# Kernel tuning notes

Hardware: AMD Instinct MI355X
Metric: run time of the kernel (lower is better)

## Reference

```python
import jax, jax.numpy as jnp
import numpy as np

B, S, D = 4, 2048, 1024
H, HD = 16, 64  # nb_heads, head_size


def setup_inputs() -> dict:
    key = jax.random.key(0)
    ks = jax.random.split(key, 9)
    s = 1.0 / np.sqrt(D)
    return {
        "x": jax.random.normal(ks[0], (B, S, D), dtype=jnp.float32),
        "wq": jax.random.uniform(ks[1], (D, D), jnp.float32, -s, s),
        "bq": jax.random.uniform(ks[2], (D,), jnp.float32, -s, s),
        "wk": jax.random.uniform(ks[3], (D, D), jnp.float32, -s, s),
        "bk": jax.random.uniform(ks[4], (D,), jnp.float32, -s, s),
        "wv": jax.random.uniform(ks[5], (D, D), jnp.float32, -s, s),
        "bv": jax.random.uniform(ks[6], (D,), jnp.float32, -s, s),
        "wo": jax.random.uniform(ks[7], (D, D), jnp.float32, -s, s),
        "bo": jax.random.uniform(ks[8], (D,), jnp.float32, -s, s),
    }


def _split_heads(t):
    # [B,S,D] -> [B,H,S,HD]
    return t.reshape(B, S, H, HD).transpose(0, 2, 1, 3)


def reference(x, wq, bq, wk, bk, wv, bv, wo, bo):
    q = _split_heads(x @ wq + bq)
    k = _split_heads(x @ wk + bk)
    v = _split_heads(x @ wv + bv)
    scores = jnp.einsum("bhqd,bhkd->bhqk", q, k) / jnp.sqrt(jnp.float32(HD))
    causal = jnp.tril(jnp.ones((S, S), dtype=bool))
    scores = jnp.where(causal, scores, -jnp.inf)
    w = jax.nn.softmax(scores, axis=-1)
    a = jnp.einsum("bhqk,bhkd->bhqd", w, v)
    a = a.transpose(0, 2, 1, 3).reshape(B, S, D)
    return a @ wo + bo
```

## Files before the change

### kernel.cpp

```cpp
#include <hip/hip_runtime.h>
#include <hip/hip_bf16.h>

typedef __bf16 bf16;
typedef bf16 bf16x8 __attribute__((ext_vector_type(8)));
typedef float f32x4 __attribute__((ext_vector_type(4)));
typedef unsigned short u16;

#define B_ 4
#define S_ 2048
#define D_ 1024
#define H_ 16
#define HD_ 64

#define NEG_SENT -30000.0f

#define XN_OFF   ((size_t)0)
#define WT_OFF   ((size_t)8388608)
#define BN_OFF   ((size_t)12582912)
#define FLAG_BYTE ((size_t)25174016)
#define Q_OFF    ((size_t)12587520)
#define K_OFF    ((size_t)20976128)
#define VT_OFF   ((size_t)29364736)

union Pack4 { bf16 b[4]; uint2 q; };

__device__ __forceinline__ void load16(const bf16* g, bf16* l) {
    __builtin_amdgcn_global_load_lds(
        (const __attribute__((address_space(1))) void*)g,
        (__attribute__((address_space(3))) void*)l, 16, 0, 0);
}

__global__ __launch_bounds__(256) void preproc_k(
    const void* __restrict__ x,
    const void* __restrict__ W0, const void* __restrict__ W1,
    const void* __restrict__ W2, const void* __restrict__ W3,
    const void* __restrict__ b0, const void* __restrict__ b1,
    const void* __restrict__ b2, const void* __restrict__ b3,
    bf16* __restrict__ XN, bf16* __restrict__ WT, bf16* __restrict__ BN,
    int* __restrict__ flag)
{
    __shared__ __align__(16) bf16 tile[64][65];
    __shared__ int cnt;
    const int t = threadIdx.x;
    const int bid = blockIdx.x;

    if (t == 0) cnt = 0;
    __syncthreads();
    {
        const u16* xs = (const u16*)x;
        int c = 0;
        for (int i = t; i < 4096; i += 256) {
            u16 w = xs[i * 2];
            int e = (w >> 7) & 0xFF;
            if (e >= 100 && e <= 135) c++;
        }
        atomicAdd(&cnt, c);
    }
    __syncthreads();
    const int isb = (cnt > 2048) ? 1 : 0;

    if (bid < 2048) {
        for (int qi = bid * 256 + t; qi < 2097152; qi += 2048 * 256) {
            if (isb) {
                ((uint2*)XN)[qi] = ((const uint2*)x)[qi];
            } else {
                float4 v = ((const float4*)x)[qi];
                Pack4 p;
                p.b[0] = (bf16)v.x; p.b[1] = (bf16)v.y;
                p.b[2] = (bf16)v.z; p.b[3] = (bf16)v.w;
                ((uint2*)XN)[qi] = p.q;
            }
        }
    } else if (bid < 3072) {
        const int idx = bid - 2048;
        const int mat = idx >> 8;
        const int rem = idx & 255;
        const int r0 = ((rem >> 4) & 15) * 64, c0 = (rem & 15) * 64;
        const void* W = (mat == 0) ? W0 : (mat == 1) ? W1
                        : (mat == 2) ? W2 : W3;
        bf16* O = WT + ((size_t)mat << 20);
        #pragma unroll
        for (int i = 0; i < 16; ++i) {
            int id2 = t + i * 256;
            int r = id2 >> 6, c = id2 & 63;
            size_t off = (size_t)(r0 + r) * D_ + c0 + c;
            tile[r][c] = isb ? ((const bf16*)W)[off]
                             : (bf16)((const float*)W)[off];
        }
        __syncthreads();
        #pragma unroll
        for (int i = 0; i < 16; ++i) {
            int id2 = t + i * 256;
            int rr = id2 & 63, cc = id2 >> 6;
            O[(size_t)(c0 + cc) * D_ + r0 + rr] = tile[rr][cc];
        }
    } else {
        if (t == 0) *flag = isb;
        const int i = t * 4;
        #pragma unroll
        for (int mat = 0; mat < 4; ++mat) {
            const void* src = (mat == 0) ? b0 : (mat == 1) ? b1
                              : (mat == 2) ? b2 : b3;
            bf16* dst = BN + mat * 1024;
            if (isb) {
                ((uint2*)(dst + i))[0] = *(const uint2*)((const bf16*)src + i);
            } else {
                const float* s = (const float*)src;
                Pack4 p;
                p.b[0] = (bf16)s[i + 0]; p.b[1] = (bf16)s[i + 1];
                p.b[2] = (bf16)s[i + 2]; p.b[3] = (bf16)s[i + 3];
                ((uint2*)(dst + i))[0] = p.q;
            }
        }
    }
}

__device__ __forceinline__ void gemm_core(const bf16* __restrict__ A,
                                          const bf16* __restrict__ Bt,
                                          bf16* lA, bf16* lB,
                                          f32x4 acc[4][4], int m0, int n0)
{
    const int t = threadIdx.x;
    const int lane = t & 63;
    const int wave = t >> 6;
    const int wm = (wave >> 1) << 6;
    const int wn = (wave & 1) << 6;
    const int quad = lane >> 4;
    const int col = lane & 15;
    for (int k0 = 0; k0 < D_; k0 += 32) {
        #pragma unroll
        for (int i = 0; i < 2; ++i) {
            int slot = t + i * 256;
            int row = slot >> 2;
            int kc = (slot & 3) << 3;
            load16(A + (size_t)(m0 + row) * D_ + k0 + kc, lA + slot * 8);
            load16(Bt + (size_t)(n0 + row) * D_ + k0 + kc, lB + slot * 8);
        }
        __syncthreads();
        bf16x8 af[4], bfr[4];
        #pragma unroll
        for (int mi = 0; mi < 4; ++mi)
            af[mi] = *(const bf16x8*)(lA + (wm + mi * 16 + col) * 32 + quad * 8);
        #pragma unroll
        for (int ni = 0; ni < 4; ++ni)
            bfr[ni] = *(const bf16x8*)(lB + (wn + ni * 16 + col) * 32 + quad * 8);
        #pragma unroll
        for (int mi = 0; mi < 4; ++mi)
            #pragma unroll
            for (int ni = 0; ni < 4; ++ni)
                acc[mi][ni] = __builtin_amdgcn_mfma_f32_16x16x32_bf16(
                    af[mi], bfr[ni], acc[mi][ni], 0, 0, 0);
        __syncthreads();
    }
}

__global__ __launch_bounds__(256) void gemm_qkv_k(
    const bf16* __restrict__ X, const bf16* __restrict__ WT,
    const bf16* __restrict__ BN,
    bf16* __restrict__ Qo, bf16* __restrict__ Ko, bf16* __restrict__ Vo)
{
    __shared__ __align__(16) bf16 lA[128 * 32];
    __shared__ __align__(16) bf16 lB[128 * 32];
    const int mode = blockIdx.z;
    const bf16* Wsel = WT + ((size_t)mode << 20);
    const bf16* bias = BN + mode * 1024;
    f32x4 acc[4][4];
    const f32x4 z = {0.f, 0.f, 0.f, 0.f};
    #pragma unroll
    for (int i = 0; i < 4; ++i)
        #pragma unroll
        for (int j = 0; j < 4; ++j) acc[i][j] = z;
    const int m0 = blockIdx.x * 128, n0 = blockIdx.y * 128;
    gemm_core(X, Wsel, lA, lB, acc, m0, n0);
    const int t = threadIdx.x, lane = t & 63, wave = t >> 6;
    const int wm = (wave >> 1) << 6, wn = (wave & 1) << 6;
    const int quad = lane >> 4, col = lane & 15;
    const float scale = (mode == 0) ? 0.18033688011112042f : 1.0f;
    #pragma unroll
    for (int mi = 0; mi < 4; ++mi) {
        int gm = m0 + wm + mi * 16 + quad * 4;
        int b = gm >> 11, srow = gm & 2047;
        #pragma unroll
        for (int ni = 0; ni < 4; ++ni) {
            int gn = n0 + wn + ni * 16 + col;
            float bb = (float)bias[gn];
            int h = gn >> 6, hd = gn & 63;
            if (mode == 2) {
                Pack4 pk;
                #pragma unroll
                for (int r = 0; r < 4; ++r)
                    pk.b[r] = (bf16)(acc[mi][ni][r] + bb);
                *(uint2*)(Vo + (((size_t)b * H_ + h) * HD_ + hd) * S_ + srow)
                    = pk.q;
            } else {
                #pragma unroll
                for (int r = 0; r < 4; ++r) {
                    float v = (acc[mi][ni][r] + bb) * scale;
                    if (mode == 1)
                        Ko[(((size_t)b * H_ + h) * S_ + srow + r) * HD_ + hd] = (bf16)v;
                    else
                        Qo[(((size_t)b * H_ + h) * S_ + srow + r) * HD_ + hd] = (bf16)v;
                }
            }
        }
    }
}

__device__ __forceinline__ void tile_step(
    const bf16* __restrict__ lK, const bf16* __restrict__ lV,
    bf16* __restrict__ lPTw,
    const bf16x8 qf[2], const bf16x8 vf4,
    f32x4 o[4], f32x4& o4, float& mst,
    int k0, int wq0)
{
    const int lane = threadIdx.x & 63;
    const int quad = lane >> 4, col = lane & 15;
    const f32x4 z = {0.f, 0.f, 0.f, 0.f};
    bool inc[4];
    inc[0] = true;
    inc[1] = (k0 + 16 <= wq0 + 15);
    inc[2] = (k0 + 32 <= wq0 + 15);
    inc[3] = (k0 + 48 <= wq0 + 15);
    f32x4 st[4];
    #pragma unroll
    for (int mt = 0; mt < 4; ++mt) st[mt] = z;
    __builtin_amdgcn_s_setprio(1);
    #pragma unroll
    for (int cc = 0; cc < 2; ++cc) {
        #pragma unroll
        for (int mt = 0; mt < 4; ++mt)
            if (inc[mt]) {
                bf16x8 af = *(const bf16x8*)(lK + (mt * 16 + col) * 64
                            + (((cc * 4 + quad) ^ (col & 7)) << 3));
                st[mt] = __builtin_amdgcn_mfma_f32_16x16x32_bf16(
                    af, qf[cc], st[mt], 0, 0, 0);
            }
    }
    __builtin_amdgcn_s_setprio(0);
    if (k0 + 64 > wq0) {
        #pragma unroll
        for (int mt = 0; mt < 4; ++mt)
            if (inc[mt]) {
                #pragma unroll
                for (int r = 0; r < 4; ++r)
                    if (k0 + mt * 16 + quad * 4 + r > wq0 + col)
                        st[mt][r] = NEG_SENT;
            }
    }
    float tm = fmaxf(fmaxf(st[0][0], st[0][1]), fmaxf(st[0][2], st[0][3]));
    #pragma unroll
    for (int mt = 1; mt < 4; ++mt)
        if (inc[mt])
            tm = fmaxf(tm, fmaxf(fmaxf(st[mt][0], st[mt][1]),
                                 fmaxf(st[mt][2], st[mt][3])));
    tm = fmaxf(tm, __shfl_xor(tm, 16));
    tm = fmaxf(tm, __shfl_xor(tm, 32));
    if (!__all(tm <= mst + 8.0f)) {
        float mn = fmaxf(mst, tm);
        float al = exp2f(mst - mn);
        #pragma unroll
        for (int dt = 0; dt < 4; ++dt) o[dt] *= al;
        o4 *= al;
        mst = mn;
    }
    #pragma unroll
    for (int mt = 0; mt < 4; ++mt) {
        int kch = mt * 2 + (quad >> 1);
        uint2* dst = (uint2*)(&lPTw[col * 64 + ((kch ^ (col & 7)) << 3)
                                    + ((quad & 1) << 2)]);
        if (inc[mt]) {
            Pack4 pk;
            #pragma unroll
            for (int r = 0; r < 4; ++r)
                pk.b[r] = (bf16)exp2f(st[mt][r] - mst);
            *dst = pk.q;
        } else if (mt == 1 || (mt == 3 && inc[2])) {
            uint2 zz; zz.x = 0u; zz.y = 0u;
            *dst = zz;
        }
    }
    asm volatile("s_waitcnt lgkmcnt(0)" ::: "memory");
    __builtin_amdgcn_s_setprio(1);
    #pragma unroll
    for (int kk = 0; kk < 2; ++kk) {
        if (kk == 1 && !inc[2]) continue;
        bf16x8 pf = *(const bf16x8*)(&lPTw[col * 64
                    + (((kk * 4 + quad) ^ (col & 7)) << 3)]);
        #pragma unroll
        for (int dt = 0; dt < 4; ++dt) {
            bf16x8 vf = *(const bf16x8*)(lV + (dt * 16 + col) * 64
                        + (((kk * 4 + quad) ^ (col & 7)) << 3));
            o[dt] = __builtin_amdgcn_mfma_f32_16x16x32_bf16(
                vf, pf, o[dt], 0, 0, 0);
        }
        o4 = __builtin_amdgcn_mfma_f32_16x16x32_bf16(vf4, pf, o4, 0, 0, 0);
    }
    __builtin_amdgcn_s_setprio(0);
}

__device__ __forceinline__ void tile_epilogue(
    bf16* __restrict__ Aout, int b, int h, int wq0,
    const f32x4 o[4], const f32x4& o4)
{
    const int lane = threadIdx.x & 63;
    const int quad = lane >> 4, col = lane & 15;
    float l = __shfl(o4[0], col);
    const float inv = 1.f / fmaxf(l, 1e-30f);
    const int qg = wq0 + col;
    #pragma unroll
    for (int dt = 0; dt < 4; ++dt) {
        Pack4 pk;
        #pragma unroll
        for (int r = 0; r < 4; ++r) pk.b[r] = (bf16)(o[dt][r] * inv);
        *(uint2*)(Aout + ((size_t)b * S_ + qg) * D_ + h * HD_
                  + dt * 16 + quad * 4) = pk.q;
    }
}

__global__ __launch_bounds__(256, 4) void attn_k(
    const bf16* __restrict__ Q, const bf16* __restrict__ K,
    const bf16* __restrict__ VT, bf16* __restrict__ Aout)
{
    __shared__ __align__(16) bf16 lK[2][64 * 64];
    __shared__ __align__(16) bf16 lV[2][64 * 64];
    __shared__ __align__(16) bf16 lPT[4][16 * 64];
    const int bh = blockIdx.y;
    const bf16* Qp = Q + (size_t)bh * S_ * HD_;
    const bf16* Kp = K + (size_t)bh * S_ * HD_;
    const bf16* Vp = VT + (size_t)bh * HD_ * S_;
    const int b = bh >> 4, h = bh & 15;
    const int t = threadIdx.x;
    const int lane = t & 63, w = t >> 6;
    const int quad = lane >> 4, col = lane & 15;
    bf16* lPTw = &lPT[w][0];

    const int q0L = (31 - (int)blockIdx.x) * 64;
    const int q0S = (int)blockIdx.x * 64;
    const int wq0L = q0L + w * 16, wq0S = q0S + w * 16;
    const int nt = 32 - (int)blockIdx.x;

    bf16x8 qfL[2], qfS[2];
    #pragma unroll
    for (int cc = 0; cc < 2; ++cc) {
        qfL[cc] = *(const bf16x8*)(Qp + (size_t)(wq0L + col) * HD_
                                   + cc * 32 + quad * 8);
        qfS[cc] = *(const bf16x8*)(Qp + (size_t)(wq0S + col) * HD_
                                   + cc * 32 + quad * 8);
    }
    const bf16 ov = (bf16)(col == 0 ? 1.0f : 0.0f);
    const bf16x8 vf4 = {ov, ov, ov, ov, ov, ov, ov, ov};

    f32x4 oL[4], oS[4], o4L, o4S;
    const f32x4 z = {0.f, 0.f, 0.f, 0.f};
    #pragma unroll
    for (int dt = 0; dt < 4; ++dt) { oL[dt] = z; oS[dt] = z; }
    o4L = z; o4S = z;
    float mstL = NEG_SENT, mstS = NEG_SENT;

    auto stage = [&](int k0, int bb) {
        #pragma unroll
        for (int i = 0; i < 2; ++i) {
            int slot = t + i * 256;
            int rr = slot >> 3, ch = slot & 7;
            int sw = (ch ^ (rr & 7)) << 3;
            load16(Kp + (size_t)(k0 + rr) * HD_ + sw, &lK[bb][slot * 8]);
            load16(Vp + (size_t)rr * S_ + k0 + sw, &lV[bb][slot * 8]);
        }
    };

    stage(0, 0);
    __syncthreads();
    int cur = 0;

    for (int it = 0; it < nt; ++it) {
        const int k0 = it << 6;
        if (it + 1 < nt) stage(k0 + 64, cur ^ 1);
        tile_step(&lK[cur][0], &lV[cur][0], lPTw, qfL, vf4,
                  oL, o4L, mstL, k0, wq0L);
        if (k0 <= q0S)
            tile_step(&lK[cur][0], &lV[cur][0], lPTw, qfS, vf4,
                      oS, o4S, mstS, k0, wq0S);
        __syncthreads();
        cur ^= 1;
    }

    tile_epilogue(Aout, b, h, wq0L, oL, o4L);
    tile_epilogue(Aout, b, h, wq0S, oS, o4S);
}

__global__ __launch_bounds__(256) void gemm_out_k(
    const bf16* __restrict__ A, const bf16* __restrict__ WoT,
    const bf16* __restrict__ Bo, void* __restrict__ Out,
    const int* __restrict__ flag)
{
    __shared__ __align__(16) bf16 lA[128 * 32];
    __shared__ __align__(16) bf16 lB[128 * 32];
    f32x4 acc[4][4];
    const f32x4 z = {0.f, 0.f, 0.f, 0.f};
    #pragma unroll
    for (int i = 0; i < 4; ++i)
        #pragma unroll
        for (int j = 0; j < 4; ++j) acc[i][j] = z;
    const int m0 = blockIdx.x * 128, n0 = blockIdx.y * 128;
    gemm_core(A, WoT, lA, lB, acc, m0, n0);
    const int t = threadIdx.x, lane = t & 63, wave = t >> 6;
    const int wm = (wave >> 1) << 6, wn = (wave & 1) << 6;
    const int quad = lane >> 4, col = lane & 15;
    const int isb = *flag;
    #pragma unroll
    for (int mi = 0; mi < 4; ++mi) {
        int gm = m0 + wm + mi * 16 + quad * 4;
        #pragma unroll
        for (int ni = 0; ni < 4; ++ni) {
            int gn = n0 + wn + ni * 16 + col;
            float bb = (float)Bo[gn];
            #pragma unroll
            for (int r = 0; r < 4; ++r) {
                float v = acc[mi][ni][r] + bb;
                size_t off = (size_t)(gm + r) * D_ + gn;
                if (isb) ((bf16*)Out)[off] = (bf16)v;
                else     ((float*)Out)[off] = v;
            }
        }
    }
}

extern "C" void kernel_launch(void* const* d_in, const int* in_sizes, int n_in,
                              void* d_out, int out_size, void* d_ws, size_t ws_size,
                              hipStream_t stream)
{
    const void* x  = d_in[0];
    const void* wq = d_in[1];
    const void* bq = d_in[2];
    const void* wk = d_in[3];
    const void* bk = d_in[4];
    const void* wv = d_in[5];
    const void* bv = d_in[6];
    const void* wo = d_in[7];
    const void* bo = d_in[8];

    bf16* ws  = (bf16*)d_ws;
    bf16* XN  = ws + XN_OFF;
    bf16* WT  = ws + WT_OFF;
    bf16* BN  = ws + BN_OFF;
    int*  flag = (int*)((char*)d_ws + FLAG_BYTE);
    bf16* Qb  = ws + Q_OFF;
    bf16* Kb  = ws + K_OFF;
    bf16* VTb = ws + VT_OFF;
    bf16* Ab  = XN;

    hipLaunchKernelGGL(preproc_k, dim3(3073), dim3(256), 0, stream,
                       x, wq, wk, wv, wo, bq, bk, bv, bo,
                       XN, WT, BN, flag);
    hipLaunchKernelGGL(gemm_qkv_k, dim3(64, 8, 3), dim3(256), 0, stream,
                       XN, WT, BN, Qb, Kb, VTb);
    hipLaunchKernelGGL(attn_k, dim3(16, 64), dim3(256), 0, stream,
                       Qb, Kb, VTb, Ab);
    hipLaunchKernelGGL(gemm_out_k, dim3(64, 8), dim3(256), 0, stream,
                       Ab, WT + ((size_t)3u << 20), BN + 3072, d_out, flag);
}
```

Measured before the change: 288.4 us.

## Interleave long and short query tiles to share K/V LDS fragment loads

Each attention iteration now processes the long and short query tiles together instead of running tile_step twice. Each K and V fragment read from LDS feeds MFMAs for both tiles, and the two sets of independent MFMAs are interleaved for more instruction-level parallelism. The P buffer is doubled per wave so both tiles' probabilities stay live, and launch bounds drop from 4 to 3 blocks per CU to allow the extra registers. The cost is higher register and LDS pressure and lower occupancy.

```diff
diff --git a/kernel.cpp b/kernel.cpp
--- a/kernel.cpp
+++ b/kernel.cpp
@@ -206,37 +206,12 @@
     }
 }
 
-__device__ __forceinline__ void tile_step(
-    const bf16* __restrict__ lK, const bf16* __restrict__ lV,
-    bf16* __restrict__ lPTw,
-    const bf16x8 qf[2], const bf16x8 vf4,
-    f32x4 o[4], f32x4& o4, float& mst,
-    int k0, int wq0)
+__device__ __forceinline__ void softmax_store(
+    f32x4 st[4], const bool inc[4], int k0, int wq0,
+    float& mst, f32x4 o[4], f32x4& o4, bf16* __restrict__ lPTw)
 {
     const int lane = threadIdx.x & 63;
     const int quad = lane >> 4, col = lane & 15;
-    const f32x4 z = {0.f, 0.f, 0.f, 0.f};
-    bool inc[4];
-    inc[0] = true;
-    inc[1] = (k0 + 16 <= wq0 + 15);
-    inc[2] = (k0 + 32 <= wq0 + 15);
-    inc[3] = (k0 + 48 <= wq0 + 15);
-    f32x4 st[4];
-    #pragma unroll
-    for (int mt = 0; mt < 4; ++mt) st[mt] = z;
-    __builtin_amdgcn_s_setprio(1);
-    #pragma unroll
-    for (int cc = 0; cc < 2; ++cc) {
-        #pragma unroll
-        for (int mt = 0; mt < 4; ++mt)
-            if (inc[mt]) {
-                bf16x8 af = *(const bf16x8*)(lK + (mt * 16 + col) * 64
-                            + (((cc * 4 + quad) ^ (col & 7)) << 3));
-                st[mt] = __builtin_amdgcn_mfma_f32_16x16x32_bf16(
-                    af, qf[cc], st[mt], 0, 0, 0);
-            }
-    }
-    __builtin_amdgcn_s_setprio(0);
     if (k0 + 64 > wq0) {
         #pragma unroll
         for (int mt = 0; mt < 4; ++mt)
@@ -279,23 +254,6 @@
             *dst = zz;
         }
     }
-    asm volatile("s_waitcnt lgkmcnt(0)" ::: "memory");
-    __builtin_amdgcn_s_setprio(1);
-    #pragma unroll
-    for (int kk = 0; kk < 2; ++kk) {
-        if (kk == 1 && !inc[2]) continue;
-        bf16x8 pf = *(const bf16x8*)(&lPTw[col * 64
-                    + (((kk * 4 + quad) ^ (col & 7)) << 3)]);
-        #pragma unroll
-        for (int dt = 0; dt < 4; ++dt) {
-            bf16x8 vf = *(const bf16x8*)(lV + (dt * 16 + col) * 64
-                        + (((kk * 4 + quad) ^ (col & 7)) << 3));
-            o[dt] = __builtin_amdgcn_mfma_f32_16x16x32_bf16(
-                vf, pf, o[dt], 0, 0, 0);
-        }
-        o4 = __builtin_amdgcn_mfma_f32_16x16x32_bf16(vf4, pf, o4, 0, 0, 0);
-    }
-    __builtin_amdgcn_s_setprio(0);
 }
 
 __device__ __forceinline__ void tile_epilogue(
@@ -317,13 +275,13 @@
     }
 }
 
-__global__ __launch_bounds__(256, 4) void attn_k(
+__global__ __launch_bounds__(256, 3) void attn_k(
     const bf16* __restrict__ Q, const bf16* __restrict__ K,
     const bf16* __restrict__ VT, bf16* __restrict__ Aout)
 {
     __shared__ __align__(16) bf16 lK[2][64 * 64];
     __shared__ __align__(16) bf16 lV[2][64 * 64];
-    __shared__ __align__(16) bf16 lPT[4][16 * 64];
+    __shared__ __align__(16) bf16 lPT[4][2][16 * 64];
     const int bh = blockIdx.y;
     const bf16* Qp = Q + (size_t)bh * S_ * HD_;
     const bf16* Kp = K + (size_t)bh * S_ * HD_;
@@ -332,7 +290,6 @@
     const int t = threadIdx.x;
     const int lane = t & 63, w = t >> 6;
     const int quad = lane >> 4, col = lane & 15;
-    bf16* lPTw = &lPT[w][0];
 
     const int q0L = (31 - (int)blockIdx.x) * 64;
     const int q0S = (int)blockIdx.x * 64;
@@ -375,11 +332,75 @@
     for (int it = 0; it < nt; ++it) {
         const int k0 = it << 6;
         if (it + 1 < nt) stage(k0 + 64, cur ^ 1);
-        tile_step(&lK[cur][0], &lV[cur][0], lPTw, qfL, vf4,
-                  oL, o4L, mstL, k0, wq0L);
-        if (k0 <= q0S)
-            tile_step(&lK[cur][0], &lV[cur][0], lPTw, qfS, vf4,
-                      oS, o4S, mstS, k0, wq0S);
+        const bf16* K_ = &lK[cur][0];
+        const bf16* V_ = &lV[cur][0];
+        const bool doS = (k0 <= q0S);
+
+        bool incL[4], incS[4];
+        #pragma unroll
+        for (int mt = 0; mt < 4; ++mt) {
+            incL[mt] = (k0 + mt * 16 <= wq0L + 15);
+            incS[mt] = (k0 + mt * 16 <= wq0S + 15);
+        }
+
+        f32x4 stL[4], stS[4];
+        #pragma unroll
+        for (int mt = 0; mt < 4; ++mt) { stL[mt] = z; stS[mt] = z; }
+        __builtin_amdgcn_s_setprio(1);
+        #pragma unroll
+        for (int cc = 0; cc < 2; ++cc) {
+            #pragma unroll
+            for (int mt = 0; mt < 4; ++mt)
+                if (incL[mt]) {
+                    bf16x8 af = *(const bf16x8*)(K_ + (mt * 16 + col) * 64
+                                + (((cc * 4 + quad) ^ (col & 7)) << 3));
+                    stL[mt] = __builtin_amdgcn_mfma_f32_16x16x32_bf16(
+                        af, qfL[cc], stL[mt], 0, 0, 0);
+                    if (doS && incS[mt])
+                        stS[mt] = __builtin_amdgcn_mfma_f32_16x16x32_bf16(
+                            af, qfS[cc], stS[mt], 0, 0, 0);
+                }
+        }
+        __builtin_amdgcn_s_setprio(0);
+
+        softmax_store(stL, incL, k0, wq0L, mstL, oL, o4L, &lPT[w][0][0]);
+        if (doS)
+            softmax_store(stS, incS, k0, wq0S, mstS, oS, o4S, &lPT[w][1][0]);
+        asm volatile("s_waitcnt lgkmcnt(0)" ::: "memory");
+
+        __builtin_amdgcn_s_setprio(1);
+        #pragma unroll
+        for (int kk = 0; kk < 2; ++kk) {
+            const bool needL = (kk == 0) ? true : incL[2];
+            const bool needS = doS && ((kk == 0) ? true : incS[2]);
+            if (!needL && !needS) continue;
+            bf16x8 pfL_, pfS_;
+            if (needL)
+                pfL_ = *(const bf16x8*)(&lPT[w][0][col * 64
+                        + (((kk * 4 + quad) ^ (col & 7)) << 3)]);
+            if (needS)
+                pfS_ = *(const bf16x8*)(&lPT[w][1][col * 64
+                        + (((kk * 4 + quad) ^ (col & 7)) << 3)]);
+            #pragma unroll
+            for (int dt = 0; dt < 4; ++dt) {
+                bf16x8 vf = *(const bf16x8*)(V_ + (dt * 16 + col) * 64
+                            + (((kk * 4 + quad) ^ (col & 7)) << 3));
+                if (needL)
+                    oL[dt] = __builtin_amdgcn_mfma_f32_16x16x32_bf16(
+                        vf, pfL_, oL[dt], 0, 0, 0);
+                if (needS)
+                    oS[dt] = __builtin_amdgcn_mfma_f32_16x16x32_bf16(
+                        vf, pfS_, oS[dt], 0, 0, 0);
+            }
+            if (needL)
+                o4L = __builtin_amdgcn_mfma_f32_16x16x32_bf16(
+                    vf4, pfL_, o4L, 0, 0, 0);
+            if (needS)
+                o4S = __builtin_amdgcn_mfma_f32_16x16x32_bf16(
+                    vf4, pfS_, o4S, 0, 0, 0);
+        }
+        __builtin_amdgcn_s_setprio(0);
+
         __syncthreads();
         cur ^= 1;
     }
```

Result: slower. 888.3 us (+208.0%).

## Split long and short causal query tiles across separate wave groups

Applied to the files above, without the earlier changes.

The attention kernel goes from 256 to 512 threads. The first four waves handle the long causal query tile and the last four handle the short one, where before each wave processed both tiles one after the other. The shared K/V staging is now spread over all 512 threads, one 16-byte load per thread per tensor. This halves the serial work and register state per wave and adds wave-level parallelism. In exchange, the short-tile waves sit idle at barriers once their causal range ends, and the larger block with 4 blocks per SM requested may limit occupancy or cause register spills.

```diff
diff --git a/kernel.cpp b/kernel.cpp
--- a/kernel.cpp
+++ b/kernel.cpp
@@ -317,13 +317,13 @@
     }
 }
 
-__global__ __launch_bounds__(256, 4) void attn_k(
+__global__ __launch_bounds__(512, 4) void attn_k(
     const bf16* __restrict__ Q, const bf16* __restrict__ K,
     const bf16* __restrict__ VT, bf16* __restrict__ Aout)
 {
     __shared__ __align__(16) bf16 lK[2][64 * 64];
     __shared__ __align__(16) bf16 lV[2][64 * 64];
-    __shared__ __align__(16) bf16 lPT[4][16 * 64];
+    __shared__ __align__(16) bf16 lPT[8][16 * 64];
     const int bh = blockIdx.y;
     const bf16* Qp = Q + (size_t)bh * S_ * HD_;
     const bf16* Kp = K + (size_t)bh * S_ * HD_;
@@ -331,41 +331,38 @@
     const int b = bh >> 4, h = bh & 15;
     const int t = threadIdx.x;
     const int lane = t & 63, w = t >> 6;
+    const int grp = w >> 2;
+    const int wl = w & 3;
     const int quad = lane >> 4, col = lane & 15;
     bf16* lPTw = &lPT[w][0];
 
     const int q0L = (31 - (int)blockIdx.x) * 64;
     const int q0S = (int)blockIdx.x * 64;
-    const int wq0L = q0L + w * 16, wq0S = q0S + w * 16;
+    const int q0  = grp ? q0S : q0L;
+    const int wq0 = q0 + wl * 16;
     const int nt = 32 - (int)blockIdx.x;
 
-    bf16x8 qfL[2], qfS[2];
-    #pragma unroll
-    for (int cc = 0; cc < 2; ++cc) {
-        qfL[cc] = *(const bf16x8*)(Qp + (size_t)(wq0L + col) * HD_
-                                   + cc * 32 + quad * 8);
-        qfS[cc] = *(const bf16x8*)(Qp + (size_t)(wq0S + col) * HD_
-                                   + cc * 32 + quad * 8);
-    }
+    bf16x8 qf[2];
+    #pragma unroll
+    for (int cc = 0; cc < 2; ++cc)
+        qf[cc] = *(const bf16x8*)(Qp + (size_t)(wq0 + col) * HD_
+                                  + cc * 32 + quad * 8);
     const bf16 ov = (bf16)(col == 0 ? 1.0f : 0.0f);
     const bf16x8 vf4 = {ov, ov, ov, ov, ov, ov, ov, ov};
 
-    f32x4 oL[4], oS[4], o4L, o4S;
+    f32x4 o[4], o4;
     const f32x4 z = {0.f, 0.f, 0.f, 0.f};
     #pragma unroll
-    for (int dt = 0; dt < 4; ++dt) { oL[dt] = z; oS[dt] = z; }
-    o4L = z; o4S = z;
-    float mstL = NEG_SENT, mstS = NEG_SENT;
+    for (int dt = 0; dt < 4; ++dt) o[dt] = z;
+    o4 = z;
+    float mst = NEG_SENT;
 
     auto stage = [&](int k0, int bb) {
-        #pragma unroll
-        for (int i = 0; i < 2; ++i) {
-            int slot = t + i * 256;
-            int rr = slot >> 3, ch = slot & 7;
-            int sw = (ch ^ (rr & 7)) << 3;
-            load16(Kp + (size_t)(k0 + rr) * HD_ + sw, &lK[bb][slot * 8]);
-            load16(Vp + (size_t)rr * S_ + k0 + sw, &lV[bb][slot * 8]);
-        }
+        int slot = t;
+        int rr = slot >> 3, ch = slot & 7;
+        int sw = (ch ^ (rr & 7)) << 3;
+        load16(Kp + (size_t)(k0 + rr) * HD_ + sw, &lK[bb][slot * 8]);
+        load16(Vp + (size_t)rr * S_ + k0 + sw, &lV[bb][slot * 8]);
     };
 
     stage(0, 0);
@@ -375,17 +372,14 @@
     for (int it = 0; it < nt; ++it) {
         const int k0 = it << 6;
         if (it + 1 < nt) stage(k0 + 64, cur ^ 1);
-        tile_step(&lK[cur][0], &lV[cur][0], lPTw, qfL, vf4,
-                  oL, o4L, mstL, k0, wq0L);
-        if (k0 <= q0S)
-            tile_step(&lK[cur][0], &lV[cur][0], lPTw, qfS, vf4,
-                      oS, o4S, mstS, k0, wq0S);
+        if (k0 <= q0)
+            tile_step(&lK[cur][0], &lV[cur][0], lPTw, qf, vf4,
+                      o, o4, mst, k0, wq0);
         __syncthreads();
         cur ^= 1;
     }
 
-    tile_epilogue(Aout, b, h, wq0L, oL, o4L);
-    tile_epilogue(Aout, b, h, wq0S, oS, o4S);
+    tile_epilogue(Aout, b, h, wq0, o, o4);
 }
 
 __global__ __launch_bounds__(256) void gemm_out_k(
@@ -454,7 +448,7 @@
                        XN, WT, BN, flag);
     hipLaunchKernelGGL(gemm_qkv_k, dim3(64, 8, 3), dim3(256), 0, stream,
                        XN, WT, BN, Qb, Kb, VTb);
-    hipLaunchKernelGGL(attn_k, dim3(16, 64), dim3(256), 0, stream,
+    hipLaunchKernelGGL(attn_k, dim3(16, 64), dim3(512), 0, stream,
                        Qb, Kb, VTb, Ab);
     hipLaunchKernelGGL(gemm_out_k, dim3(64, 8), dim3(256), 0, stream,
                        Ab, WT + ((size_t)3u << 20), BN + 3072, d_out, flag);
```

After: 319.1 us. +10.6%, slower.
